# Optimization experiments

Measured on AMD Instinct MI355X. Metric: run time of the kernel, lower is better.

## Reference

```python
import jax, jax.numpy as jnp
import numpy as np

M_DIM, Z_DIM, C = 256, 128, 32
N, L = 512, 384


def setup_inputs() -> dict:
    key = jax.random.key(0)
    ks = jax.random.split(key, 9)
    s = 1.0 / np.sqrt(M_DIM)
    return {
        "m": jax.random.normal(ks[0], (N, L, M_DIM), dtype=jnp.float32),
        "ln_gamma": jnp.ones((M_DIM,), jnp.float32),
        "ln_beta": jnp.zeros((M_DIM,), jnp.float32),
        "w1": jax.random.normal(ks[1], (M_DIM, C), jnp.float32) * s,
        "b1": jnp.zeros((C,), jnp.float32),
        "w2": jax.random.normal(ks[2], (M_DIM, C), jnp.float32) * s,
        "b2": jnp.zeros((C,), jnp.float32),
        "w3": jax.random.normal(ks[3], (C * C, Z_DIM), jnp.float32) * (1.0 / np.sqrt(C * C)),
        "b3": jnp.zeros((Z_DIM,), jnp.float32),
    }


def _layernorm(x, gamma, beta, eps=1e-5):
    mu = jnp.mean(x, axis=-1, keepdims=True)
    var = jnp.mean(jnp.square(x - mu), axis=-1, keepdims=True)
    return (x - mu) * jax.lax.rsqrt(var + eps) * gamma + beta


def reference(m, ln_gamma, ln_beta, w1, b1, w2, b2, w3, b3):
    n = m.shape[0]
    o = _layernorm(m, ln_gamma, ln_beta)          # (N, L, D)
    a = o @ w2 + b2                                # (N, L, C)  linear2
    b = o @ w1 + b1                                # (N, L, C)  linear1
    # mean over N of outer products: reassociated as a single contraction over n
    op = jnp.einsum('nia,njb->ijab', a, b) / n     # (L, L, C, C)
    ll = op.shape[0]
    z = op.reshape(ll, ll, -1) @ w3 + b3           # (L, L, Z)
    return z
```

## Files before the change

### kernel.cpp

```cpp
#include <hip/hip_runtime.h>
#include <hip/hip_bf16.h>
#include <stdint.h>

#define L_DIM 384
#define MD    256
#define CC    32
#define ZD    128
#define NB    512
#define K2    1024
#define MROWS 12288

typedef __attribute__((ext_vector_type(4))) float  f32x4;
typedef __attribute__((ext_vector_type(8))) short  bf16x8;

typedef __attribute__((address_space(1))) unsigned char* gcp;
typedef __attribute__((address_space(3))) unsigned char* lcp;

#define SBAR()  __builtin_amdgcn_s_barrier()
#define LGKM0() asm volatile("s_waitcnt lgkmcnt(0)" ::: "memory")
#define VMW(n)  asm volatile("s_waitcnt vmcnt(" #n ")" ::: "memory")
#define PRIO1() __builtin_amdgcn_s_setprio(1)
#define PRIO0() __builtin_amdgcn_s_setprio(0)

__device__ __forceinline__ unsigned short f2bf(float x) {
    union { float f; unsigned u; } v; v.f = x;
    unsigned r = v.u + 0x7fffu + ((v.u >> 16) & 1u);
    return (unsigned short)(r >> 16);
}

__device__ __forceinline__ uint2 pack4(unsigned short a, unsigned short b,
                                       unsigned short c, unsigned short d) {
    uint2 r; r.x = (unsigned)a | ((unsigned)b << 16);
    r.y = (unsigned)c | ((unsigned)d << 16); return r;
}

__global__ __launch_bounds__(256) void prep_kernel(
    const float* __restrict__ w1, const float* __restrict__ w2,
    const float* __restrict__ w3,
    unsigned short* __restrict__ w3frag, unsigned short* __restrict__ wfrag)
{
    int idx = blockIdx.x * 256 + threadIdx.x;
    if (idx < 131072) {
        int e = idx & 7, lane = (idx >> 3) & 63, zg = (idx >> 9) & 7, ks = idx >> 12;
        int k2 = ks * 32 + ((lane >> 4) << 3) + e;
        int z  = zg * 16 + (lane & 15);
        w3frag[idx] = f2bf(w3[(size_t)k2 * ZD + z]);
    } else {
        int j = idx - 131072;
        int e = j & 7, lane = (j >> 3) & 63, nf = (j >> 9) & 3, ks = j >> 11;
        int c = nf * 16 + (lane & 15);
        int d = ks * 32 + ((lane >> 4) << 3) + e;
        float v = (c < CC) ? w2[d * CC + c] : w1[d * CC + (c - CC)];
        wfrag[j] = f2bf(v);
    }
}

__global__ __launch_bounds__(256, 4) void ln_proj_kernel(
    const float* __restrict__ mm, const float* __restrict__ gamma, const float* __restrict__ beta,
    const unsigned short* __restrict__ wfrag,
    const float* __restrict__ b1, const float* __restrict__ b2,
    unsigned short* __restrict__ At, unsigned short* __restrict__ Bt)
{
    __shared__ alignas(16) char o_b[32768];

    const int tid = threadIdx.x, wv = tid >> 6, lane = tid & 63;
    const int l0 = blockIdx.y * 2;
    const int n0 = blockIdx.x * 32;

    const int l_loc = wv >> 1;
    const int nbase = (wv & 1) << 4;
    const int l_g = l0 + l_loc;
    f32x4 g4 = *(const f32x4*)(gamma + lane * 4);
    f32x4 e4 = *(const f32x4*)(beta + lane * 4);

    #pragma unroll 4
    for (int r = 0; r < 16; ++r) {
        int row_loc = wv * 16 + r;
        int n_g = n0 + nbase + r;
        const float* src = mm + ((size_t)n_g * L_DIM + l_g) * MD + lane * 4;
        f32x4 x = *(const f32x4*)src;
        float s  = x[0] + x[1] + x[2] + x[3];
        float s2 = x[0]*x[0] + x[1]*x[1] + x[2]*x[2] + x[3]*x[3];
        #pragma unroll
        for (int off = 32; off > 0; off >>= 1) {
            s  += __shfl_xor(s,  off);
            s2 += __shfl_xor(s2, off);
        }
        float mu  = s * (1.0f / MD);
        float var = s2 * (1.0f / MD) - mu * mu;
        float rs  = rsqrtf(var + 1e-5f);
        unsigned short o0 = f2bf((x[0] - mu) * rs * g4[0] + e4[0]);
        unsigned short o1 = f2bf((x[1] - mu) * rs * g4[1] + e4[1]);
        unsigned short o2 = f2bf((x[2] - mu) * rs * g4[2] + e4[2]);
        unsigned short o3 = f2bf((x[3] - mu) * rs * g4[3] + e4[3]);
        *(uint2*)(o_b + row_loc * 512 + ((lane * 8) ^ ((row_loc & 7) << 4))) = pack4(o0, o1, o2, o3);
    }

    f32x4 acc[4] = {{0,0,0,0},{0,0,0,0},{0,0,0,0},{0,0,0,0}};
    const int lrow = lane & 15;
    const int kq16 = (lane >> 4) << 4;
    const int arow = wv * 16 + lrow;
    #pragma unroll
    for (int ks = 0; ks < 8; ++ks) {
        bf16x8 a = *(const bf16x8*)(o_b + arow * 512 + ((ks * 64 + kq16) ^ ((arow & 7) << 4)));
        #pragma unroll
        for (int nf = 0; nf < 4; ++nf) {
            bf16x8 b = *(const bf16x8*)(wfrag + (size_t)((ks * 4 + nf) * 64 + lane) * 8);
            acc[nf] = __builtin_amdgcn_mfma_f32_16x16x32_bf16(a, b, acc[nf], 0, 0, 0);
        }
    }

    const int rr0 = wv * 16 + ((lane >> 4) << 2);
    const int n_gw = n0 + (rr0 & 31);
    const int l_gw = l0 + (rr0 >> 5);
    #pragma unroll
    for (int nf = 0; nf < 4; ++nf) {
        int c = nf * 16 + lrow;
        float bias = (c < CC) ? b2[c] : b1[c - CC];
        unsigned short ob0 = f2bf(acc[nf][0] + bias);
        unsigned short ob1 = f2bf(acc[nf][1] + bias);
        unsigned short ob2 = f2bf(acc[nf][2] + bias);
        unsigned short ob3 = f2bf(acc[nf][3] + bias);
        unsigned short* dst = ((c < CC) ? At : Bt) + (size_t)(l_gw * CC + (c & 31)) * NB + n_gw;
        *(uint2*)dst = pack4(ob0, ob1, ob2, ob3);
    }
}

__global__ __launch_bounds__(512, 2) void opm_kernel(
    const unsigned short* __restrict__ At, const unsigned short* __restrict__ Bt,
    const unsigned short* __restrict__ w3frag, const float* __restrict__ b3,
    float* __restrict__ Z)
{
    __shared__ alignas(128) char smem[131072];
    char* const Ab = smem;
    char* const Bb = smem + 65536;

    const int tid = threadIdx.x, wv = tid >> 6, lane = tid & 63;
    const int i0 = blockIdx.x * 256, j0 = blockIdx.y * 256;
    const int lrow = lane & 15;
    const int kq16 = (lane >> 4) << 4;
    const int wr = (wv >> 2) * 128, wc = (wv & 3) * 64;

    auto stage = [&](const unsigned short* __restrict__ src, int tile0, int kt,
                     int half, int isA) {
        #pragma unroll
        for (int q = 0; q < 2; ++q) {
            int rl0 = q * 64 + wv * 8;
            int rl  = rl0 + (lane >> 3);
            int rc  = isA ? ((rl  & 63) + ((rl  >> 6) << 7) + half * 64)
                          : ((rl  & 31) + ((rl  >> 5) << 6) + half * 32);
            int rc0 = isA ? ((rl0 & 63) + ((rl0 >> 6) << 7) + half * 64)
                          : ((rl0 & 31) + ((rl0 >> 5) << 6) + half * 32);
            const unsigned short* g = src + (size_t)(tile0 + rc) * NB + kt * 64
                                      + (((lane & 7) ^ (lane >> 3)) << 3);
            char* l = (isA ? Ab : Bb) + (kt & 1) * 32768 + rc0 * 128;
            __builtin_amdgcn_global_load_lds((gcp)g, (lcp)l, 16, 0, 0);
        }
    };

    f32x4 acc[8][4] = {};
    bf16x8 av[8], bl[4], bh[4];

    auto rdA = [&](const char* ab, int qrow) {
        #pragma unroll
        for (int mfl = 0; mfl < 4; ++mfl) {
            int row = wr + qrow * 64 + mfl * 16 + lrow;
            const char* p = ab + row * 128;
            av[mfl*2+0] = *(const bf16x8*)(p + ((     kq16) ^ ((row & 7) << 4)));
            av[mfl*2+1] = *(const bf16x8*)(p + ((64 + kq16) ^ ((row & 7) << 4)));
        }
    };
    auto rdB = [&](const char* bb, int qcol, bf16x8* bv) {
        #pragma unroll
        for (int nfl = 0; nfl < 2; ++nfl) {
            int col = wc + qcol * 32 + nfl * 16 + lrow;
            const char* p = bb + col * 128;
            bv[nfl*2+0] = *(const bf16x8*)(p + ((     kq16) ^ ((col & 7) << 4)));
            bv[nfl*2+1] = *(const bf16x8*)(p + ((64 + kq16) ^ ((col & 7) << 4)));
        }
    };
    auto MM = [&](bf16x8* bv, int mbase, int nbase) {
        #pragma unroll
        for (int mfl = 0; mfl < 4; ++mfl)
            #pragma unroll
            for (int nfl = 0; nfl < 2; ++nfl)
                #pragma unroll
                for (int ks = 0; ks < 2; ++ks)
                    acc[mbase+mfl][nbase+nfl] = __builtin_amdgcn_mfma_f32_16x16x32_bf16(
                        av[mfl*2+ks], bv[nfl*2+ks], acc[mbase+mfl][nbase+nfl], 0, 0, 0);
    };

    stage(At, i0, 0, 0, 1); stage(At, i0, 0, 1, 1);
    stage(Bt, j0, 0, 0, 0); stage(Bt, j0, 0, 1, 0);
    stage(At, i0, 1, 0, 1); stage(At, i0, 1, 1, 1);
    stage(Bt, j0, 1, 0, 0); stage(Bt, j0, 1, 1, 0);
    VMW(8);
    SBAR();

    for (int t = 0; t < 4; ++t) {
        const int ktc = (2*t + 2) & 7, ktd = (2*t + 3) & 7;
        const char* a0 = Ab;           const char* b0 = Bb;
        const char* a1 = Ab + 32768;   const char* b1 = Bb + 32768;
        rdA(a0, 0); rdB(b0, 0, bl);
        SBAR(); LGKM0(); PRIO1(); MM(bl, 0, 0); PRIO0(); SBAR();
        rdB(b0, 1, bh); stage(At, i0, ktc, 0, 1);
        SBAR(); LGKM0(); PRIO1(); MM(bh, 0, 2); PRIO0(); SBAR();
        rdA(a0, 1); stage(Bt, j0, ktc, 0, 0);
        SBAR(); LGKM0(); PRIO1(); MM(bh, 4, 2); PRIO0(); SBAR();
        stage(Bt, j0, ktc, 1, 0);
        SBAR(); LGKM0(); PRIO1(); MM(bl, 4, 0); PRIO0(); VMW(6); SBAR();
        rdA(a1, 0); rdB(b1, 0, bl); stage(At, i0, ktc, 1, 1);
        SBAR(); LGKM0(); PRIO1(); MM(bl, 0, 0); PRIO0(); SBAR();
        rdB(b1, 1, bh); stage(At, i0, ktd, 0, 1);
        SBAR(); LGKM0(); PRIO1(); MM(bh, 0, 2); PRIO0(); SBAR();
        rdA(a1, 1); stage(Bt, j0, ktd, 0, 0);
        SBAR(); LGKM0(); PRIO1(); MM(bh, 4, 2); PRIO0(); SBAR();
        stage(Bt, j0, ktd, 1, 0); stage(At, i0, ktd, 1, 1);
        SBAR(); LGKM0(); PRIO1(); MM(bl, 4, 0); PRIO0(); VMW(8); SBAR();
    }

    VMW(0);
    __syncthreads();

    char* const opb = smem;
    const float scale = 1.0f / (float)NB;
    #pragma unroll
    for (int mf = 0; mf < 8; ++mf) {
        #pragma unroll
        for (int nf = 0; nf < 4; ++nf) {
            int col = wc + nf * 16 + lrow;
            #pragma unroll
            for (int rr = 0; rr < 4; ++rr) {
                int row = wr + mf * 16 + ((lane >> 4) << 2) + rr;
                int pl = ((row >> 5) << 3) | (col >> 5);
                int k2 = ((row & 31) << 5) | (col & 31);
                *(unsigned short*)(opb + pl * 2048 + ((k2 * 2) ^ ((pl & 7) << 4))) =
                    f2bf(acc[mf][nf][rr] * scale);
            }
        }
    }
    __syncthreads();

    f32x4 acc2[2][2] = {};
    const int pfb = (wv >> 2) * 2, zgb = (wv & 3) * 2;
    const int row0 = pfb * 16 + lrow, row1 = row0 + 16;
    #pragma unroll 4
    for (int ks = 0; ks < 32; ++ks) {
        int g = ks * 4 + (lane >> 4);
        bf16x8 p0 = *(const bf16x8*)(opb + row0 * 2048 + ((g * 16) ^ ((row0 & 7) << 4)));
        bf16x8 p1 = *(const bf16x8*)(opb + row1 * 2048 + ((g * 16) ^ ((row1 & 7) << 4)));
        bf16x8 w0 = *(const bf16x8*)(w3frag + (size_t)((ks * 8 + zgb    ) * 64 + lane) * 8);
        bf16x8 w1 = *(const bf16x8*)(w3frag + (size_t)((ks * 8 + zgb + 1) * 64 + lane) * 8);
        acc2[0][0] = __builtin_amdgcn_mfma_f32_16x16x32_bf16(p0, w0, acc2[0][0], 0, 0, 0);
        acc2[0][1] = __builtin_amdgcn_mfma_f32_16x16x32_bf16(p0, w1, acc2[0][1], 0, 0, 0);
        acc2[1][0] = __builtin_amdgcn_mfma_f32_16x16x32_bf16(p1, w0, acc2[1][0], 0, 0, 0);
        acc2[1][1] = __builtin_amdgcn_mfma_f32_16x16x32_bf16(p1, w1, acc2[1][1], 0, 0, 0);
    }

    #pragma unroll
    for (int p = 0; p < 2; ++p) {
        #pragma unroll
        for (int zi = 0; zi < 2; ++zi) {
            int zc = (zgb + zi) * 16 + lrow;
            float bias = b3[zc];
            #pragma unroll
            for (int rr = 0; rr < 4; ++rr) {
                int pl = (pfb + p) * 16 + ((lane >> 4) << 2) + rr;
                int ii = blockIdx.x * 8 + (pl >> 3);
                int jj = blockIdx.y * 8 + (pl & 7);
                Z[((size_t)ii * L_DIM + jj) * ZD + zc] = acc2[p][zi][rr] + bias;
            }
        }
    }
}

extern "C" void kernel_launch(void* const* d_in, const int* in_sizes, int n_in,
                              void* d_out, int out_size, void* d_ws, size_t ws_size,
                              hipStream_t stream)
{
    const float* mm    = (const float*)d_in[0];
    const float* gamma = (const float*)d_in[1];
    const float* beta  = (const float*)d_in[2];
    const float* w1    = (const float*)d_in[3];
    const float* b1    = (const float*)d_in[4];
    const float* w2    = (const float*)d_in[5];
    const float* b2    = (const float*)d_in[6];
    const float* w3    = (const float*)d_in[7];
    const float* b3    = (const float*)d_in[8];

    unsigned short* At     = (unsigned short*)d_ws;
    unsigned short* Bt     = At + (size_t)MROWS * NB;
    unsigned short* w3frag = Bt + (size_t)MROWS * NB;
    unsigned short* wfrag  = w3frag + 131072;

    prep_kernel<<<576, 256, 0, stream>>>(w1, w2, w3, w3frag, wfrag);
    ln_proj_kernel<<<dim3(16, 192), 256, 0, stream>>>(mm, gamma, beta, wfrag, b1, b2, At, Bt);
    opm_kernel<<<dim3(48, 48), 512, 0, stream>>>(At, Bt, w3frag, b3, (float*)d_out);
}
```

Before: 279.5 us.

## Peel GEMM tail, vectorize op stores, software-pipeline W3 GEMM, swizzle blocks across XCDs

Remaps block indices so that blocks sharing the same i-range land on the same XCD, for better L2 reuse of At and Bt. Peels the last K iteration of the main GEMM so no redundant stage loads are issued for wrapped tiles. The outer-product tile is now written to LDS transposed ((b,a) order, matched by a permuted w3frag layout) as packed 8-byte stores instead of scalar 2-byte stores. The second GEMM is software-pipelined with register double-buffering of the P and W loads. This adds register pressure and more complex swizzle indexing.

```diff
diff --git a/kernel.cpp b/kernel.cpp
--- a/kernel.cpp
+++ b/kernel.cpp
@@ -42,9 +42,10 @@
     int idx = blockIdx.x * 256 + threadIdx.x;
     if (idx < 131072) {
         int e = idx & 7, lane = (idx >> 3) & 63, zg = (idx >> 9) & 7, ks = idx >> 12;
-        int k2 = ks * 32 + ((lane >> 4) << 3) + e;
+        int k2p = ks * 32 + ((lane >> 4) << 3) + e;
+        int wrow = (k2p & 31) * 32 + (k2p >> 5);
         int z  = zg * 16 + (lane & 15);
-        w3frag[idx] = f2bf(w3[(size_t)k2 * ZD + z]);
+        w3frag[idx] = f2bf(w3[(size_t)wrow * ZD + z]);
     } else {
         int j = idx - 131072;
         int e = j & 7, lane = (j >> 3) & 63, nf = (j >> 9) & 3, ks = j >> 11;
@@ -136,7 +137,12 @@
     char* const Bb = smem + 65536;
 
     const int tid = threadIdx.x, wv = tid >> 6, lane = tid & 63;
-    const int i0 = blockIdx.x * 256, j0 = blockIdx.y * 256;
+
+    const int lin = blockIdx.y * 48 + blockIdx.x;
+    const int xcd = lin & 7, chunk = lin >> 3;
+    const int i0 = (xcd * 6 + (chunk % 6)) * 256;
+    const int j0 = (chunk / 6) * 256;
+
     const int lrow = lane & 15;
     const int kq16 = (lane >> 4) << 4;
     const int wr = (wv >> 2) * 128, wc = (wv & 3) * 64;
@@ -197,10 +203,11 @@
     VMW(8);
     SBAR();
 
-    for (int t = 0; t < 4; ++t) {
-        const int ktc = (2*t + 2) & 7, ktd = (2*t + 3) & 7;
-        const char* a0 = Ab;           const char* b0 = Bb;
-        const char* a1 = Ab + 32768;   const char* b1 = Bb + 32768;
+    const char* a0 = Ab;           const char* b0 = Bb;
+    const char* a1 = Ab + 32768;   const char* b1 = Bb + 32768;
+
+    for (int t = 0; t < 3; ++t) {
+        const int ktc = 2*t + 2, ktd = 2*t + 3;
         rdA(a0, 0); rdB(b0, 0, bl);
         SBAR(); LGKM0(); PRIO1(); MM(bl, 0, 0); PRIO0(); SBAR();
         rdB(b0, 1, bh); stage(At, i0, ktc, 0, 1);
@@ -219,44 +226,84 @@
         SBAR(); LGKM0(); PRIO1(); MM(bl, 4, 0); PRIO0(); VMW(8); SBAR();
     }
 
-    VMW(0);
-    __syncthreads();
+    rdA(a0, 0); rdB(b0, 0, bl);
+    SBAR(); LGKM0(); PRIO1(); MM(bl, 0, 0); PRIO0(); SBAR();
+    rdB(b0, 1, bh);
+    SBAR(); LGKM0(); PRIO1(); MM(bh, 0, 2); PRIO0(); SBAR();
+    rdA(a0, 1);
+    SBAR(); LGKM0(); PRIO1(); MM(bh, 4, 2); PRIO0(); SBAR();
+    SBAR(); LGKM0(); PRIO1(); MM(bl, 4, 0); PRIO0(); VMW(0); SBAR();
+    rdA(a1, 0); rdB(b1, 0, bl);
+    SBAR(); LGKM0(); PRIO1(); MM(bl, 0, 0); PRIO0(); SBAR();
+    rdB(b1, 1, bh);
+    SBAR(); LGKM0(); PRIO1(); MM(bh, 0, 2); PRIO0(); SBAR();
+    rdA(a1, 1);
+    SBAR(); LGKM0(); PRIO1(); MM(bh, 4, 2); PRIO0(); SBAR();
+    SBAR(); LGKM0(); PRIO1(); MM(bl, 4, 0); PRIO0(); SBAR();
 
     char* const opb = smem;
+    const int pfb = (wv >> 2) * 2, zgb = (wv & 3) * 2;
+    const int row0 = pfb * 16 + lrow, row1 = row0 + 16;
+    const int lq = lane >> 4;
+
+    auto ldW = [&](int ks, int zg) -> bf16x8 {
+        return *(const bf16x8*)(w3frag + (size_t)((ks * 8 + zg) * 64 + lane) * 8);
+    };
+    auto ldP = [&](int row, int ks) -> bf16x8 {
+        int g = ks * 4 + lq;
+        int b = g >> 2, jj = g & 3;
+        int inner = (b * 64 + jj * 16) ^ (((b >> 1) & 7) << 4) ^ ((row & 7) << 4);
+        return *(const bf16x8*)(opb + row * 2048 + inner);
+    };
+
+    bf16x8 wA0 = ldW(0, zgb), wA1 = ldW(0, zgb + 1);
+    bf16x8 wB0 = ldW(1, zgb), wB1 = ldW(1, zgb + 1);
+
     const float scale = 1.0f / (float)NB;
     #pragma unroll
     for (int mf = 0; mf < 8; ++mf) {
         #pragma unroll
         for (int nf = 0; nf < 4; ++nf) {
             int col = wc + nf * 16 + lrow;
-            #pragma unroll
-            for (int rr = 0; rr < 4; ++rr) {
-                int row = wr + mf * 16 + ((lane >> 4) << 2) + rr;
-                int pl = ((row >> 5) << 3) | (col >> 5);
-                int k2 = ((row & 31) << 5) | (col & 31);
-                *(unsigned short*)(opb + pl * 2048 + ((k2 * 2) ^ ((pl & 7) << 4))) =
-                    f2bf(acc[mf][nf][rr] * scale);
-            }
+            int b = col & 31;
+            int row = wr + mf * 16 + ((lane >> 4) << 2);
+            int pl = ((row >> 5) << 3) | (col >> 5);
+            int a0e = row & 31;
+            int inner = (b * 64 + a0e * 2) ^ (((b >> 1) & 7) << 4) ^ ((pl & 7) << 4);
+            *(uint2*)(opb + pl * 2048 + inner) =
+                pack4(f2bf(acc[mf][nf][0] * scale), f2bf(acc[mf][nf][1] * scale),
+                      f2bf(acc[mf][nf][2] * scale), f2bf(acc[mf][nf][3] * scale));
         }
     }
     __syncthreads();
 
     f32x4 acc2[2][2] = {};
-    const int pfb = (wv >> 2) * 2, zgb = (wv & 3) * 2;
-    const int row0 = pfb * 16 + lrow, row1 = row0 + 16;
-    #pragma unroll 4
-    for (int ks = 0; ks < 32; ++ks) {
-        int g = ks * 4 + (lane >> 4);
-        bf16x8 p0 = *(const bf16x8*)(opb + row0 * 2048 + ((g * 16) ^ ((row0 & 7) << 4)));
-        bf16x8 p1 = *(const bf16x8*)(opb + row1 * 2048 + ((g * 16) ^ ((row1 & 7) << 4)));
-        bf16x8 w0 = *(const bf16x8*)(w3frag + (size_t)((ks * 8 + zgb    ) * 64 + lane) * 8);
-        bf16x8 w1 = *(const bf16x8*)(w3frag + (size_t)((ks * 8 + zgb + 1) * 64 + lane) * 8);
-        acc2[0][0] = __builtin_amdgcn_mfma_f32_16x16x32_bf16(p0, w0, acc2[0][0], 0, 0, 0);
-        acc2[0][1] = __builtin_amdgcn_mfma_f32_16x16x32_bf16(p0, w1, acc2[0][1], 0, 0, 0);
-        acc2[1][0] = __builtin_amdgcn_mfma_f32_16x16x32_bf16(p1, w0, acc2[1][0], 0, 0, 0);
-        acc2[1][1] = __builtin_amdgcn_mfma_f32_16x16x32_bf16(p1, w1, acc2[1][1], 0, 0, 0);
-    }
-
+    bf16x8 pA0 = ldP(row0, 0), pA1 = ldP(row1, 0);
+    bf16x8 pB0 = ldP(row0, 1), pB1 = ldP(row1, 1);
+    for (int ks = 0; ks < 32; ks += 2) {
+        bf16x8 wN0 = {}, wN1 = {}, pN0 = {}, pN1 = {};
+        bf16x8 wM0 = {}, wM1 = {}, pM0 = {}, pM1 = {};
+        if (ks + 2 < 32) {
+            wN0 = ldW(ks + 2, zgb); wN1 = ldW(ks + 2, zgb + 1);
+            pN0 = ldP(row0, ks + 2); pN1 = ldP(row1, ks + 2);
+            wM0 = ldW(ks + 3, zgb); wM1 = ldW(ks + 3, zgb + 1);
+            pM0 = ldP(row0, ks + 3); pM1 = ldP(row1, ks + 3);
+        }
+        PRIO1();
+        acc2[0][0] = __builtin_amdgcn_mfma_f32_16x16x32_bf16(pA0, wA0, acc2[0][0], 0, 0, 0);
+        acc2[0][1] = __builtin_amdgcn_mfma_f32_16x16x32_bf16(pA0, wA1, acc2[0][1], 0, 0, 0);
+        acc2[1][0] = __builtin_amdgcn_mfma_f32_16x16x32_bf16(pA1, wA0, acc2[1][0], 0, 0, 0);
+        acc2[1][1] = __builtin_amdgcn_mfma_f32_16x16x32_bf16(pA1, wA1, acc2[1][1], 0, 0, 0);
+        acc2[0][0] = __builtin_amdgcn_mfma_f32_16x16x32_bf16(pB0, wB0, acc2[0][0], 0, 0, 0);
+        acc2[0][1] = __builtin_amdgcn_mfma_f32_16x16x32_bf16(pB0, wB1, acc2[0][1], 0, 0, 0);
+        acc2[1][0] = __builtin_amdgcn_mfma_f32_16x16x32_bf16(pB1, wB0, acc2[1][0], 0, 0, 0);
+        acc2[1][1] = __builtin_amdgcn_mfma_f32_16x16x32_bf16(pB1, wB1, acc2[1][1], 0, 0, 0);
+        PRIO0();
+        wA0 = wN0; wA1 = wN1; pA0 = pN0; pA1 = pN1;
+        wB0 = wM0; wB1 = wM1; pB0 = pM0; pB1 = pM1;
+    }
+
+    const int pq = (lane >> 4) << 2;
     #pragma unroll
     for (int p = 0; p < 2; ++p) {
         #pragma unroll
@@ -265,9 +312,9 @@
             float bias = b3[zc];
             #pragma unroll
             for (int rr = 0; rr < 4; ++rr) {
-                int pl = (pfb + p) * 16 + ((lane >> 4) << 2) + rr;
-                int ii = blockIdx.x * 8 + (pl >> 3);
-                int jj = blockIdx.y * 8 + (pl & 7);
+                int pl = (pfb + p) * 16 + pq + rr;
+                int ii = (i0 >> 5) + (pl >> 3);
+                int jj = (j0 >> 5) + (pl & 7);
                 Z[((size_t)ii * L_DIM + jj) * ZD + zc] = acc2[p][zi][rr] + bias;
             }
         }
```

Measured after the change: 258.2 us. 7.6% less time.

## Shrink OPM tile to 128x256 with triple-buffered K=32 pipeline and XCD-aware mapping

Applied to the files above, without the earlier changes.

The outer-product kernel moves from 256x256 tiles with double-buffered K=64 stages to 128x256 tiles with a three-slot K=32 ring buffer. This cuts LDS use from 128 KB to 72 KB, so more blocks fit per CU. Block indices are remapped so each XCD gets a contiguous band of i rows for L2 reuse. The w3 fragment layout is permuted to match a new transposed, swizzled LDS layout for the bf16 outer product, and the second GEMM software-prefetches its operands. The risks are less register reuse per tile, more barriers per K step, and a layout change that has to stay consistent between prep_kernel and opm_kernel.

```diff
diff --git a/kernel.cpp b/kernel.cpp
--- a/kernel.cpp
+++ b/kernel.cpp
@@ -10,14 +10,13 @@
 #define K2    1024
 #define MROWS 12288
 
-typedef __attribute__((ext_vector_type(4))) float  f32x4;
-typedef __attribute__((ext_vector_type(8))) short  bf16x8;
+typedef __attribute__((ext_vector_type(4)))  float f32x4;
+typedef __attribute__((ext_vector_type(8)))  short bf16x8;
 
 typedef __attribute__((address_space(1))) unsigned char* gcp;
 typedef __attribute__((address_space(3))) unsigned char* lcp;
 
 #define SBAR()  __builtin_amdgcn_s_barrier()
-#define LGKM0() asm volatile("s_waitcnt lgkmcnt(0)" ::: "memory")
 #define VMW(n)  asm volatile("s_waitcnt vmcnt(" #n ")" ::: "memory")
 #define PRIO1() __builtin_amdgcn_s_setprio(1)
 #define PRIO0() __builtin_amdgcn_s_setprio(0)
@@ -42,9 +41,10 @@
     int idx = blockIdx.x * 256 + threadIdx.x;
     if (idx < 131072) {
         int e = idx & 7, lane = (idx >> 3) & 63, zg = (idx >> 9) & 7, ks = idx >> 12;
-        int k2 = ks * 32 + ((lane >> 4) << 3) + e;
+        int k2p = ks * 32 + ((lane >> 4) << 3) + e;
+        int wrow = (k2p & 31) * 32 + (k2p >> 5);
         int z  = zg * 16 + (lane & 15);
-        w3frag[idx] = f2bf(w3[(size_t)k2 * ZD + z]);
+        w3frag[idx] = f2bf(w3[(size_t)wrow * ZD + z]);
     } else {
         int j = idx - 131072;
         int e = j & 7, lane = (j >> 3) & 63, nf = (j >> 9) & 3, ks = j >> 11;
@@ -126,150 +126,142 @@
     }
 }
 
-__global__ __launch_bounds__(512, 2) void opm_kernel(
+__global__ __launch_bounds__(512, 4) void opm_kernel(
     const unsigned short* __restrict__ At, const unsigned short* __restrict__ Bt,
     const unsigned short* __restrict__ w3frag, const float* __restrict__ b3,
     float* __restrict__ Z)
 {
-    __shared__ alignas(128) char smem[131072];
-    char* const Ab = smem;
-    char* const Bb = smem + 65536;
-
+    __shared__ alignas(128) char smem[73728];
     const int tid = threadIdx.x, wv = tid >> 6, lane = tid & 63;
-    const int i0 = blockIdx.x * 256, j0 = blockIdx.y * 256;
+
+    const int lin = blockIdx.x;
+    const int xcd = lin & 7, c = lin >> 3;
+    const int i0 = (xcd * 12 + (c % 12)) * 128;
+    const int j0 = (c / 12) * 256;
+
     const int lrow = lane & 15;
-    const int kq16 = (lane >> 4) << 4;
-    const int wr = (wv >> 2) * 128, wc = (wv & 3) * 64;
-
-    auto stage = [&](const unsigned short* __restrict__ src, int tile0, int kt,
-                     int half, int isA) {
-        #pragma unroll
-        for (int q = 0; q < 2; ++q) {
-            int rl0 = q * 64 + wv * 8;
-            int rl  = rl0 + (lane >> 3);
-            int rc  = isA ? ((rl  & 63) + ((rl  >> 6) << 7) + half * 64)
-                          : ((rl  & 31) + ((rl  >> 5) << 6) + half * 32);
-            int rc0 = isA ? ((rl0 & 63) + ((rl0 >> 6) << 7) + half * 64)
-                          : ((rl0 & 31) + ((rl0 >> 5) << 6) + half * 32);
-            const unsigned short* g = src + (size_t)(tile0 + rc) * NB + kt * 64
-                                      + (((lane & 7) ^ (lane >> 3)) << 3);
-            char* l = (isA ? Ab : Bb) + (kt & 1) * 32768 + rc0 * 128;
+    const int wrB = (wv >> 2) * 64, wcB = (wv & 3) * 64;
+
+    const int f0 = wv * 3;
+    const int s_row = lane >> 2;
+    const int s_kof = ((lane & 3) ^ (s_row & 3)) << 3;
+
+    auto stage = [&](int t) {
+        const int buf = t % 3;
+        #pragma unroll
+        for (int q = 0; q < 3; ++q) {
+            int f = f0 + q;
+            const unsigned short* g;
+            char* l;
+            if (f < 8) {
+                g = At + (size_t)(i0 + f * 16 + s_row) * NB + t * 32 + s_kof;
+                l = smem + buf * 8192 + f * 1024;
+            } else {
+                g = Bt + (size_t)(j0 + (f - 8) * 16 + s_row) * NB + t * 32 + s_kof;
+                l = smem + 24576 + buf * 16384 + (f - 8) * 1024;
+            }
             __builtin_amdgcn_global_load_lds((gcp)g, (lcp)l, 16, 0, 0);
         }
     };
 
-    f32x4 acc[8][4] = {};
-    bf16x8 av[8], bl[4], bh[4];
-
-    auto rdA = [&](const char* ab, int qrow) {
-        #pragma unroll
-        for (int mfl = 0; mfl < 4; ++mfl) {
-            int row = wr + qrow * 64 + mfl * 16 + lrow;
-            const char* p = ab + row * 128;
-            av[mfl*2+0] = *(const bf16x8*)(p + ((     kq16) ^ ((row & 7) << 4)));
-            av[mfl*2+1] = *(const bf16x8*)(p + ((64 + kq16) ^ ((row & 7) << 4)));
-        }
-    };
-    auto rdB = [&](const char* bb, int qcol, bf16x8* bv) {
-        #pragma unroll
-        for (int nfl = 0; nfl < 2; ++nfl) {
-            int col = wc + qcol * 32 + nfl * 16 + lrow;
-            const char* p = bb + col * 128;
-            bv[nfl*2+0] = *(const bf16x8*)(p + ((     kq16) ^ ((col & 7) << 4)));
-            bv[nfl*2+1] = *(const bf16x8*)(p + ((64 + kq16) ^ ((col & 7) << 4)));
-        }
-    };
-    auto MM = [&](bf16x8* bv, int mbase, int nbase) {
-        #pragma unroll
-        for (int mfl = 0; mfl < 4; ++mfl)
+    f32x4 acc[4][4] = {};
+    const int rpos = ((lane >> 4) ^ (lane & 3)) << 4;
+
+    auto TILE = [&](int t) {
+        const char* ab = smem + (t % 3) * 8192;
+        const char* bb = smem + 24576 + (t % 3) * 16384;
+        bf16x8 av[4], bv[4];
+        #pragma unroll
+        for (int mf = 0; mf < 4; ++mf)
+            av[mf] = *(const bf16x8*)(ab + (wrB + mf * 16 + lrow) * 64 + rpos);
+        #pragma unroll
+        for (int nf = 0; nf < 4; ++nf)
+            bv[nf] = *(const bf16x8*)(bb + (wcB + nf * 16 + lrow) * 64 + rpos);
+        PRIO1();
+        #pragma unroll
+        for (int mf = 0; mf < 4; ++mf)
             #pragma unroll
-            for (int nfl = 0; nfl < 2; ++nfl)
-                #pragma unroll
-                for (int ks = 0; ks < 2; ++ks)
-                    acc[mbase+mfl][nbase+nfl] = __builtin_amdgcn_mfma_f32_16x16x32_bf16(
-                        av[mfl*2+ks], bv[nfl*2+ks], acc[mbase+mfl][nbase+nfl], 0, 0, 0);
-    };
-
-    stage(At, i0, 0, 0, 1); stage(At, i0, 0, 1, 1);
-    stage(Bt, j0, 0, 0, 0); stage(Bt, j0, 0, 1, 0);
-    stage(At, i0, 1, 0, 1); stage(At, i0, 1, 1, 1);
-    stage(Bt, j0, 1, 0, 0); stage(Bt, j0, 1, 1, 0);
-    VMW(8);
+            for (int nf = 0; nf < 4; ++nf)
+                acc[mf][nf] = __builtin_amdgcn_mfma_f32_16x16x32_bf16(
+                    av[mf], bv[nf], acc[mf][nf], 0, 0, 0);
+        PRIO0();
+    };
+
+    stage(0); stage(1);
+    VMW(3);
     SBAR();
 
-    for (int t = 0; t < 4; ++t) {
-        const int ktc = (2*t + 2) & 7, ktd = (2*t + 3) & 7;
-        const char* a0 = Ab;           const char* b0 = Bb;
-        const char* a1 = Ab + 32768;   const char* b1 = Bb + 32768;
-        rdA(a0, 0); rdB(b0, 0, bl);
-        SBAR(); LGKM0(); PRIO1(); MM(bl, 0, 0); PRIO0(); SBAR();
-        rdB(b0, 1, bh); stage(At, i0, ktc, 0, 1);
-        SBAR(); LGKM0(); PRIO1(); MM(bh, 0, 2); PRIO0(); SBAR();
-        rdA(a0, 1); stage(Bt, j0, ktc, 0, 0);
-        SBAR(); LGKM0(); PRIO1(); MM(bh, 4, 2); PRIO0(); SBAR();
-        stage(Bt, j0, ktc, 1, 0);
-        SBAR(); LGKM0(); PRIO1(); MM(bl, 4, 0); PRIO0(); VMW(6); SBAR();
-        rdA(a1, 0); rdB(b1, 0, bl); stage(At, i0, ktc, 1, 1);
-        SBAR(); LGKM0(); PRIO1(); MM(bl, 0, 0); PRIO0(); SBAR();
-        rdB(b1, 1, bh); stage(At, i0, ktd, 0, 1);
-        SBAR(); LGKM0(); PRIO1(); MM(bh, 0, 2); PRIO0(); SBAR();
-        rdA(a1, 1); stage(Bt, j0, ktd, 0, 0);
-        SBAR(); LGKM0(); PRIO1(); MM(bh, 4, 2); PRIO0(); SBAR();
-        stage(Bt, j0, ktd, 1, 0); stage(At, i0, ktd, 1, 1);
-        SBAR(); LGKM0(); PRIO1(); MM(bl, 4, 0); PRIO0(); VMW(8); SBAR();
-    }
-
-    VMW(0);
+    #pragma unroll
+    for (int t = 0; t < 16; ++t) {
+        if (t < 14) stage(t + 2);
+        TILE(t);
+        if (t < 14)      { VMW(3); }
+        else if (t == 14){ VMW(0); }
+        SBAR();
+    }
+
+    char* const opb = smem;
+    const int pf  = wv & 1;
+    const int zgb = (wv >> 1) * 2;
+    const int row0 = pf * 16 + lrow;
+    const int lq = lane >> 4;
+
+    auto ldW = [&](int ks, int zg) -> bf16x8 {
+        return *(const bf16x8*)(w3frag + (size_t)((ks * 8 + zg) * 64 + lane) * 8);
+    };
+    auto ldP = [&](int row, int ks) -> bf16x8 {
+        int g = ks * 4 + lq;
+        int b = g >> 2, jj = g & 3;
+        int inner = (b * 64 + jj * 16) ^ (((b >> 1) & 7) << 4) ^ ((row & 7) << 4);
+        return *(const bf16x8*)(opb + row * 2048 + inner);
+    };
+
+    bf16x8 wA0 = ldW(0, zgb), wA1 = ldW(0, zgb + 1);
+
+    const float scale = 1.0f / (float)NB;
+    #pragma unroll
+    for (int mf = 0; mf < 4; ++mf) {
+        #pragma unroll
+        for (int nf = 0; nf < 4; ++nf) {
+            int col = wcB + nf * 16 + lrow;
+            int bcol = col & 31;
+            int row = wrB + mf * 16 + ((lane >> 4) << 2);
+            int pl = ((row >> 5) << 3) | (col >> 5);
+            int a0e = row & 31;
+            int inner = (bcol * 64 + a0e * 2) ^ (((bcol >> 1) & 7) << 4) ^ ((pl & 7) << 4);
+            *(uint2*)(opb + pl * 2048 + inner) =
+                pack4(f2bf(acc[mf][nf][0] * scale), f2bf(acc[mf][nf][1] * scale),
+                      f2bf(acc[mf][nf][2] * scale), f2bf(acc[mf][nf][3] * scale));
+        }
+    }
     __syncthreads();
 
-    char* const opb = smem;
-    const float scale = 1.0f / (float)NB;
-    #pragma unroll
-    for (int mf = 0; mf < 8; ++mf) {
-        #pragma unroll
-        for (int nf = 0; nf < 4; ++nf) {
-            int col = wc + nf * 16 + lrow;
-            #pragma unroll
-            for (int rr = 0; rr < 4; ++rr) {
-                int row = wr + mf * 16 + ((lane >> 4) << 2) + rr;
-                int pl = ((row >> 5) << 3) | (col >> 5);
-                int k2 = ((row & 31) << 5) | (col & 31);
-                *(unsigned short*)(opb + pl * 2048 + ((k2 * 2) ^ ((pl & 7) << 4))) =
-                    f2bf(acc[mf][nf][rr] * scale);
-            }
-        }
-    }
-    __syncthreads();
-
-    f32x4 acc2[2][2] = {};
-    const int pfb = (wv >> 2) * 2, zgb = (wv & 3) * 2;
-    const int row0 = pfb * 16 + lrow, row1 = row0 + 16;
-    #pragma unroll 4
+    f32x4 acc2[2] = {};
+    bf16x8 pA = ldP(row0, 0);
     for (int ks = 0; ks < 32; ++ks) {
-        int g = ks * 4 + (lane >> 4);
-        bf16x8 p0 = *(const bf16x8*)(opb + row0 * 2048 + ((g * 16) ^ ((row0 & 7) << 4)));
-        bf16x8 p1 = *(const bf16x8*)(opb + row1 * 2048 + ((g * 16) ^ ((row1 & 7) << 4)));
-        bf16x8 w0 = *(const bf16x8*)(w3frag + (size_t)((ks * 8 + zgb    ) * 64 + lane) * 8);
-        bf16x8 w1 = *(const bf16x8*)(w3frag + (size_t)((ks * 8 + zgb + 1) * 64 + lane) * 8);
-        acc2[0][0] = __builtin_amdgcn_mfma_f32_16x16x32_bf16(p0, w0, acc2[0][0], 0, 0, 0);
-        acc2[0][1] = __builtin_amdgcn_mfma_f32_16x16x32_bf16(p0, w1, acc2[0][1], 0, 0, 0);
-        acc2[1][0] = __builtin_amdgcn_mfma_f32_16x16x32_bf16(p1, w0, acc2[1][0], 0, 0, 0);
-        acc2[1][1] = __builtin_amdgcn_mfma_f32_16x16x32_bf16(p1, w1, acc2[1][1], 0, 0, 0);
-    }
-
-    #pragma unroll
-    for (int p = 0; p < 2; ++p) {
-        #pragma unroll
-        for (int zi = 0; zi < 2; ++zi) {
-            int zc = (zgb + zi) * 16 + lrow;
-            float bias = b3[zc];
-            #pragma unroll
-            for (int rr = 0; rr < 4; ++rr) {
-                int pl = (pfb + p) * 16 + ((lane >> 4) << 2) + rr;
-                int ii = blockIdx.x * 8 + (pl >> 3);
-                int jj = blockIdx.y * 8 + (pl & 7);
-                Z[((size_t)ii * L_DIM + jj) * ZD + zc] = acc2[p][zi][rr] + bias;
-            }
+        bf16x8 wN0 = {}, wN1 = {}, pN = {};
+        if (ks + 1 < 32) {
+            wN0 = ldW(ks + 1, zgb); wN1 = ldW(ks + 1, zgb + 1);
+            pN  = ldP(row0, ks + 1);
+        }
+        PRIO1();
+        acc2[0] = __builtin_amdgcn_mfma_f32_16x16x32_bf16(pA, wA0, acc2[0], 0, 0, 0);
+        acc2[1] = __builtin_amdgcn_mfma_f32_16x16x32_bf16(pA, wA1, acc2[1], 0, 0, 0);
+        PRIO0();
+        wA0 = wN0; wA1 = wN1; pA = pN;
+    }
+
+    const int pq = (lane >> 4) << 2;
+    #pragma unroll
+    for (int zi = 0; zi < 2; ++zi) {
+        int zc = (zgb + zi) * 16 + lrow;
+        float bias = b3[zc];
+        #pragma unroll
+        for (int rr = 0; rr < 4; ++rr) {
+            int pl = pf * 16 + pq + rr;
+            int ii = (i0 >> 5) + (pl >> 3);
+            int jj = (j0 >> 5) + (pl & 7);
+            Z[((size_t)ii * L_DIM + jj) * ZD + zc] = acc2[zi][rr] + bias;
         }
     }
 }
@@ -295,5 +287,5 @@
 
     prep_kernel<<<576, 256, 0, stream>>>(w1, w2, w3, w3frag, wfrag);
     ln_proj_kernel<<<dim3(16, 192), 256, 0, stream>>>(mm, gamma, beta, wfrag, b1, b2, At, Bt);
-    opm_kernel<<<dim3(48, 48), 512, 0, stream>>>(At, Bt, w3frag, b3, (float*)d_out);
-}
+    opm_kernel<<<4608, 512, 0, stream>>>(At, Bt, w3frag, b3, (float*)d_out);
+}
```

Result: no change. 278.8 us (-0.2%).
